# Performance work log

Hardware: AMD Instinct MI355X
Metric: run time of the kernel (lower is better)

Reference implementation:

```python
import jax, jax.numpy as jnp
import numpy as np

SHIFT = 1  # module's random shift_direction, fixed to +1 for determinism
B, C, H, W_SP = 1024, 512, 7, 7


def setup_inputs() -> dict:
    key = jax.random.key(0)
    k1, k2 = jax.random.split(key)
    x = jax.random.normal(k1, (B, C, H, W_SP), dtype=jnp.float32)
    W = jax.random.normal(k2, (256, 3, 3, 512), dtype=jnp.float32)
    return {"x": x, "W": W}


def _forward(x, W):
    # unfold along H with kernel (3,1), padding (1,0):
    # patches[b,c,kh,h,w] = x_padded[b,c,h+kh,w]
    xp = jnp.pad(x, ((0, 0), (0, 0), (1, 1), (0, 0)))
    t2 = jnp.stack([xp[:, :, k:k + H, :] for k in range(3)], axis=2)  # (B,512,3,7,7)
    # split channels 512 -> (2,256), move group dim next to H
    t2 = t2.reshape(B, 2, 256, 3, H, W_SP)
    t2 = t2.transpose(0, 2, 3, 4, 1, 5)          # (B,256,3,7,2,7)
    t2 = t2.reshape(B, 256, 3, 14, W_SP)         # interleave (h,group) -> 14
    t2 = jnp.roll(t2, SHIFT, axis=3)             # shift along interleaved dim
    t2 = t2.reshape(B, 256, 3, 7, 2, W_SP).sum(axis=4)  # (B,256,3,7,7)
    t2 = t2.transpose(0, 1, 3, 2, 4)             # (B,256,7,3,7) = (m,l,n,j,w)
    # second shift + unfold along w with kernel 3, padding 1
    t3 = jnp.roll(t2, SHIFT, axis=4)
    tp = jnp.pad(t3, ((0, 0), (0, 0), (0, 0), (0, 0), (1, 1)))
    t3u = jnp.stack([tp[..., k:k + W_SP] for k in range(3)], axis=4)  # (B,256,7,3,3,7) = (m,l,n,j,k,p)
    # torch einsum 'mlnjok, ljki -> mnoi' with o = output position, k = kernel tap
    out = jnp.einsum('mlnjkp,ljki->mpni', t3u, W)  # wait: check axis order below
    # Note: torch permutes (m,c,h,j,kernel,pos)->(m,c,h,j,pos,kernel) before einsum,
    # so contraction is over (l,j,kernel) and output is (m, n=h, o=pos, i).
    out = jnp.einsum('mlnjkp,ljki->mnpi', t3u, W)  # (B,7,7,512)
    return out.transpose(0, 3, 1, 2)              # (B,512,7,7)


def reference(x, W):
    return _forward(x, W)
```

## Files before the change

kernel.cpp:

```cpp
#include <hip/hip_runtime.h>
#include <hip/hip_bf16.h>


typedef __bf16 bf16x8 __attribute__((ext_vector_type(8)));
typedef float f32x4 __attribute__((ext_vector_type(4)));

#define VT_OFFSET (4u << 20)
#define VT_BYTES  (7168ull * 7 * 768 * 2)
#define WS_NEED   (VT_OFFSET + VT_BYTES)

__global__ __launch_bounds__(256) void prep_w(const float* __restrict__ Wg,
                                              __bf16* __restrict__ W2) {
    __shared__ float ws_[96][65];
    const int kt = blockIdx.x % 24;
    const int it_ = blockIdx.x / 24;
    const int K0 = kt * 96;
    const int I0 = it_ * 64;
    const int tid = threadIdx.x;

    #pragma unroll
    for (int t = 0; t < 6; ++t) {
        const int u = t * 256 + tid;
        const int row = u >> 4;
        const int f4 = u & 15;
        const float4 v = *(const float4*)(Wg + (size_t)(K0 + row) * 512 + I0 + f4 * 4);
        ws_[row][f4 * 4 + 0] = v.x;
        ws_[row][f4 * 4 + 1] = v.y;
        ws_[row][f4 * 4 + 2] = v.z;
        ws_[row][f4 * 4 + 3] = v.w;
    }
    __syncthreads();

    #pragma unroll
    for (int t = 0; t < 3; ++t) {
        const int u = t * 256 + tid;
        const int i = u / 12;
        const int rem = u - i * 12;
        const int tap = rem >> 2;
        const int q = rem & 3;
        bf16x8 o;
        #pragma unroll
        for (int e = 0; e < 8; ++e) {
            const int c_loc = q * 8 + e;
            o[e] = (__bf16)ws_[3 * c_loc + tap][i];
        }
        *(bf16x8*)(W2 + (size_t)(I0 + i) * 2304 + tap * 768 + 32 * kt + q * 8) = o;
    }
}

__global__ __launch_bounds__(256) void prep_v(const float* __restrict__ x,
                                              __bf16* __restrict__ Vt) {
    __shared__ float xs[256 * 49];
    const int b = blockIdx.x >> 1;
    const int g = blockIdx.x & 1;
    const int tid = threadIdx.x;

    {
        const float4* src0 = (const float4*)(x + ((size_t)b * 512 + g * 128) * 49);
        const float4* src1 = (const float4*)(x + ((size_t)b * 512 + 256 + g * 128) * 49);
        float4* dst0 = (float4*)xs;
        float4* dst1 = (float4*)(xs + 128 * 49);
        #pragma unroll
        for (int it = 0; it < 7; ++it) {
            const int q = it * 256 + tid;
            if (q < 1568) dst0[q] = src0[q];
        }
        #pragma unroll
        for (int it = 0; it < 7; ++it) {
            const int q = it * 256 + tid;
            if (q < 1568) dst1[q] = src1[q];
        }
    }
    __syncthreads();

    for (int h = 0; h < 7; ++h) {
        const int hm = (h + 6) % 7;
        for (int it = 0; it < 2; ++it) {
            const int u = it * 256 + tid;
            if (u < 336) {
                const int r = u / 48;
                const int k = u - r * 48;
                const int w = (r + 6) % 7;
                bf16x8 vv;
                #pragma unroll
                for (int e = 0; e < 8; ++e) {
                    const int c = k * 8 + e;
                    const int l = c / 3;
                    const int j = c - 3 * l;
                    const int r1 = h + j - 1;
                    const int r2 = hm + j - 1;
                    float v = 0.f;
                    if (r1 >= 0 && r1 < 7) v += xs[l * 49 + r1 * 7 + w];
                    if (r2 >= 0 && r2 < 7) v += xs[(128 + l) * 49 + r2 * 7 + w];
                    vv[e] = (__bf16)v;
                }
                *(bf16x8*)(Vt + (size_t)((b * 7 + h) * 7 + r) * 768 + g * 384 + k * 8) = vv;
            }
        }
    }
}

__global__ __launch_bounds__(256) void gemm_vt(const __bf16* __restrict__ Vt,
                                               const __bf16* __restrict__ W2,
                                               float* __restrict__ out) {
    __shared__ __bf16 T[16 * 400];
    __shared__ __bf16 Bt[128 * 104];

    const int tid = threadIdx.x;
    const int g0 = blockIdx.x;
    const int nb = (g0 >> 3) & 3;
    const int mb = ((g0 >> 5) << 3) | (g0 & 7);
    const int i0 = nb * 128;

    for (int q = tid; q < 3200; q += 256) ((int*)T)[q] = 0;

    const int lane = tid & 63;
    const int wave = tid >> 6;
    const int wm = wave >> 1;
    const int wn = wave & 1;
    const int ln15 = lane & 15;
    const int gq = lane >> 4;

    f32x4 acc[4][4];
    #pragma unroll
    for (int a = 0; a < 4; ++a)
        #pragma unroll
        for (int bq = 0; bq < 4; ++bq) acc[a][bq] = (f32x4){0.f, 0.f, 0.f, 0.f};

    __syncthreads();

    for (int chunk = 0; chunk < 24; ++chunk) {
        #pragma unroll
        for (int it = 0; it < 2; ++it) {
            const int u = it * 256 + tid;
            if (u < 448) {
                const int q = u & 3;
                const int tmp = u >> 2;
                const int t = tmp % 7;
                const int bh = tmp / 7;
                const float4 val = *(const float4*)(
                    Vt + (size_t)((mb * 16 + bh) * 7 + t) * 768 + chunk * 32 + q * 8);
                *(float4*)(&T[bh * 400 + (t + 1) * 40 + q * 8]) = val;
            }
        }
        #pragma unroll
        for (int it = 0; it < 6; ++it) {
            const int u = it * 256 + tid;
            const int tap = u >> 9;
            const int rem = u & 511;
            const int n = rem >> 2;
            const int q = rem & 3;
            const float4 val = *(const float4*)(W2 + (size_t)(i0 + n) * 2304 +
                                                tap * 768 + chunk * 32 + q * 8);
            *(float4*)(&Bt[n * 104 + tap * 32 + q * 8]) = val;
        }

        __syncthreads();

        #pragma unroll
        for (int tap = 0; tap < 3; ++tap) {
            bf16x8 af[4], bfr[4];
            #pragma unroll
            for (int mf = 0; mf < 4; ++mf) {
                const int bh_l = wm * 8 + mf * 2 + (ln15 >> 3);
                const int p = ln15 & 7;
                af[mf] = *(const bf16x8*)(&T[(bh_l * 10 + p + tap) * 40 + gq * 8]);
            }
            #pragma unroll
            for (int nf = 0; nf < 4; ++nf) {
                const int n_l = wn * 64 + nf * 16 + ln15;
                bfr[nf] = *(const bf16x8*)(&Bt[n_l * 104 + tap * 32 + gq * 8]);
            }
            #pragma unroll
            for (int mf = 0; mf < 4; ++mf)
                #pragma unroll
                for (int nf = 0; nf < 4; ++nf)
                    acc[mf][nf] = __builtin_amdgcn_mfma_f32_16x16x32_bf16(
                        af[mf], bfr[nf], acc[mf][nf], 0, 0, 0);
        }

        __syncthreads();
    }

    #pragma unroll
    for (int mf = 0; mf < 4; ++mf) {
        #pragma unroll
        for (int r = 0; r < 4; ++r) {
            const int mrow = gq * 4 + r;
            const int Mg_l = wm * 64 + mf * 16 + mrow;
            const int p = Mg_l & 7;
            if (p == 7) continue;
            const int bh_l = Mg_l >> 3;
            const int bhg = mb * 16 + bh_l;
            const int b = bhg / 7;
            const int h = bhg - 7 * b;
            #pragma unroll
            for (int nf = 0; nf < 4; ++nf) {
                const int i = i0 + wn * 64 + nf * 16 + ln15;
                out[(((size_t)b * 512 + i) * 7 + h) * 7 + p] = acc[mf][nf][r];
            }
        }
    }
}

__global__ __launch_bounds__(256) void gemm_shift(const float* __restrict__ x,
                                                  const __bf16* __restrict__ W2,
                                                  float* __restrict__ out) {
    __shared__ __bf16 T[16 * 10 * 40];
    __shared__ __bf16 Bt[128 * 104];

    const int tid = threadIdx.x;
    const int mb = blockIdx.x >> 2;
    const int nb = blockIdx.x & 3;
    const int i0 = nb * 128;

    const int cl  = tid & 31;
    const int bh0 = tid >> 5;
    const int bhg0 = mb * 16 + bh0;
    const int bhg1 = bhg0 + 8;
    const int b0 = bhg0 / 7, h0 = bhg0 - 7 * b0;
    const int b1 = bhg1 / 7, h1 = bhg1 - 7 * b1;
    const int hm0 = (h0 + 6) % 7, hm1 = (h1 + 6) % 7;

    for (int q = tid; q < 16 * 10 * 40 / 2; q += 256) ((int*)T)[q] = 0;

    const int lane = tid & 63;
    const int wave = tid >> 6;
    const int wm = wave >> 1;
    const int wn = wave & 1;
    const int ln15 = lane & 15;
    const int gq = lane >> 4;

    f32x4 acc[4][4];
    #pragma unroll
    for (int a = 0; a < 4; ++a)
        #pragma unroll
        for (int bq = 0; bq < 4; ++bq) acc[a][bq] = (f32x4){0.f, 0.f, 0.f, 0.f};

    __syncthreads();

    for (int chunk = 0; chunk < 24; ++chunk) {
        const int cg = chunk * 32 + cl;
        const int l = cg / 3;
        const int j = cg - 3 * l;
        {
            const int r1 = h0 + j - 1, r2 = hm0 + j - 1;
            float v[7] = {0.f, 0.f, 0.f, 0.f, 0.f, 0.f, 0.f};
            if (r1 >= 0 && r1 < 7) {
                const float* p1 = x + (((size_t)b0 * 512 + l) * 7 + r1) * 7;
                #pragma unroll
                for (int w = 0; w < 7; ++w) v[w] += p1[w];
            }
            if (r2 >= 0 && r2 < 7) {
                const float* p2 = x + (((size_t)b0 * 512 + 256 + l) * 7 + r2) * 7;
                #pragma unroll
                for (int w = 0; w < 7; ++w) v[w] += p2[w];
            }
            #pragma unroll
            for (int w = 0; w < 7; ++w)
                T[bh0 * 400 + ((w + 1) % 7 + 1) * 40 + cl] = (__bf16)v[w];
        }
        {
            const int r1 = h1 + j - 1, r2 = hm1 + j - 1;
            float v[7] = {0.f, 0.f, 0.f, 0.f, 0.f, 0.f, 0.f};
            if (r1 >= 0 && r1 < 7) {
                const float* p1 = x + (((size_t)b1 * 512 + l) * 7 + r1) * 7;
                #pragma unroll
                for (int w = 0; w < 7; ++w) v[w] += p1[w];
            }
            if (r2 >= 0 && r2 < 7) {
                const float* p2 = x + (((size_t)b1 * 512 + 256 + l) * 7 + r2) * 7;
                #pragma unroll
                for (int w = 0; w < 7; ++w) v[w] += p2[w];
            }
            #pragma unroll
            for (int w = 0; w < 7; ++w)
                T[(bh0 + 8) * 400 + ((w + 1) % 7 + 1) * 40 + cl] = (__bf16)v[w];
        }

        #pragma unroll
        for (int it = 0; it < 6; ++it) {
            const int u = it * 256 + tid;
            const int tap = u >> 9;
            const int rem = u & 511;
            const int n = rem >> 2;
            const int q = rem & 3;
            const float4 val = *(const float4*)(W2 + (size_t)(i0 + n) * 2304 +
                                                tap * 768 + chunk * 32 + q * 8);
            *(float4*)(&Bt[n * 104 + tap * 32 + q * 8]) = val;
        }

        __syncthreads();

        #pragma unroll
        for (int tap = 0; tap < 3; ++tap) {
            bf16x8 af[4], bfr[4];
            #pragma unroll
            for (int mf = 0; mf < 4; ++mf) {
                const int bh_l = wm * 8 + mf * 2 + (ln15 >> 3);
                const int p = ln15 & 7;
                af[mf] = *(const bf16x8*)(&T[(bh_l * 10 + p + tap) * 40 + gq * 8]);
            }
            #pragma unroll
            for (int nf = 0; nf < 4; ++nf) {
                const int n_l = wn * 64 + nf * 16 + ln15;
                bfr[nf] = *(const bf16x8*)(&Bt[n_l * 104 + tap * 32 + gq * 8]);
            }
            #pragma unroll
            for (int mf = 0; mf < 4; ++mf)
                #pragma unroll
                for (int nf = 0; nf < 4; ++nf)
                    acc[mf][nf] = __builtin_amdgcn_mfma_f32_16x16x32_bf16(
                        af[mf], bfr[nf], acc[mf][nf], 0, 0, 0);
        }

        __syncthreads();
    }

    #pragma unroll
    for (int mf = 0; mf < 4; ++mf) {
        #pragma unroll
        for (int r = 0; r < 4; ++r) {
            const int mrow = gq * 4 + r;
            const int Mg_l = wm * 64 + mf * 16 + mrow;
            const int p = Mg_l & 7;
            if (p == 7) continue;
            const int bh_l = Mg_l >> 3;
            const int bhg = mb * 16 + bh_l;
            const int b = bhg / 7;
            const int h = bhg - 7 * b;
            #pragma unroll
            for (int nf = 0; nf < 4; ++nf) {
                const int i = i0 + wn * 64 + nf * 16 + ln15;
                out[(((size_t)b * 512 + i) * 7 + h) * 7 + p] = acc[mf][nf][r];
            }
        }
    }
}

extern "C" void kernel_launch(void* const* d_in, const int* in_sizes, int n_in,
                              void* d_out, int out_size, void* d_ws, size_t ws_size,
                              hipStream_t stream) {
    const float* x  = (const float*)d_in[0];
    const float* Wg = (const float*)d_in[1];
    float* out = (float*)d_out;
    __bf16* W2 = (__bf16*)d_ws;

    prep_w<<<dim3(192), dim3(256), 0, stream>>>(Wg, W2);

    if (ws_size >= WS_NEED) {
        __bf16* Vt = (__bf16*)((char*)d_ws + VT_OFFSET);
        prep_v<<<dim3(2048), dim3(256), 0, stream>>>(x, Vt);
        gemm_vt<<<dim3(448 * 4), dim3(256), 0, stream>>>(Vt, W2, out);
    } else {
        gemm_shift<<<dim3(448 * 4), dim3(256), 0, stream>>>(x, W2, out);
    }
}
```

Baseline: 388.9 us.

## Double-buffer gemm_vt LDS tiles with direct global-to-LDS loads and XOR swizzle

Rewrites gemm_vt's main loop to stage the next K-chunk of activations and weights straight into LDS with global_load_lds while MFMAs run on the current buffer. One barrier per chunk now guards the double buffer instead of the load-then-compute sequence. Padding columns are replaced by an XOR swizzle to avoid bank conflicts, and out-of-range taps point to a shared zero region. LDS use rises to about 62 KB per block, which may lower occupancy, and the swizzle and offset math add correctness risk.

```diff
diff --git a/kernel.cpp b/kernel.cpp
--- a/kernel.cpp
+++ b/kernel.cpp
@@ -4,10 +4,17 @@
 
 typedef __bf16 bf16x8 __attribute__((ext_vector_type(8)));
 typedef float f32x4 __attribute__((ext_vector_type(4)));
+typedef unsigned int u32;
 
 #define VT_OFFSET (4u << 20)
 #define VT_BYTES  (7168ull * 7 * 768 * 2)
 #define WS_NEED   (VT_OFFSET + VT_BYTES)
+
+__device__ __forceinline__ void gload_lds16(const void* g, void* l) {
+    __builtin_amdgcn_global_load_lds(
+        (const __attribute__((address_space(1))) u32*)g,
+        (__attribute__((address_space(3))) u32*)l, 16, 0, 0);
+}
 
 __global__ __launch_bounds__(256) void prep_w(const float* __restrict__ Wg,
                                               __bf16* __restrict__ W2) {
@@ -103,8 +110,7 @@
 __global__ __launch_bounds__(256) void gemm_vt(const __bf16* __restrict__ Vt,
                                                const __bf16* __restrict__ W2,
                                                float* __restrict__ out) {
-    __shared__ __bf16 T[16 * 400];
-    __shared__ __bf16 Bt[128 * 104];
+    __shared__ __align__(1024) char L[63616];
 
     const int tid = threadIdx.x;
     const int g0 = blockIdx.x;
@@ -112,7 +118,34 @@
     const int mb = ((g0 >> 5) << 3) | (g0 & 7);
     const int i0 = nb * 128;
 
-    for (int q = tid; q < 3200; q += 256) ((int*)T)[q] = 0;
+    if (tid < 32) {
+        const int off = (tid < 16) ? 7168 + tid * 4 : 14400 + (tid - 16) * 4;
+        *(int*)(L + off) = 0;
+    }
+
+    int tsrc[2]; bool tok[2];
+    #pragma unroll
+    for (int it = 0; it < 2; ++it) {
+        const int u = it * 256 + tid;
+        tok[it] = (u < 448);
+        const int bh = u / 28;
+        const int rem = u - bh * 28;
+        const int ct = rem >> 2;
+        const int qs = rem & 3;
+        const int q = qs ^ (ct & 3);
+        tsrc[it] = ((mb * 16 + bh) * 7 + ct) * 1536 + q * 16;
+    }
+    int bsrc[6];
+    #pragma unroll
+    for (int it = 0; it < 6; ++it) {
+        const int s = it * 256 + tid;
+        const int tap = s >> 9;
+        const int rem = s & 511;
+        const int n = rem >> 2;
+        const int qs = rem & 3;
+        const int q = qs ^ ((n >> 1) & 3);
+        bsrc[it] = ((i0 + n) * 2304 + tap * 768 + q * 8) * 2;
+    }
 
     const int lane = tid & 63;
     const int wave = tid >> 6;
@@ -121,28 +154,172 @@
     const int ln15 = lane & 15;
     const int gq = lane >> 4;
 
+    int afoff[3][4], bfoff[3][4];
+    #pragma unroll
+    for (int tap = 0; tap < 3; ++tap) {
+        #pragma unroll
+        for (int mf = 0; mf < 4; ++mf) {
+            const int bh_l = wm * 8 + mf * 2 + (ln15 >> 3);
+            const int p = ln15 & 7;
+            const int ct = p + tap - 1;
+            afoff[tap][mf] = (ct >= 0 && ct <= 6)
+                ? bh_l * 448 + ct * 64 + ((gq ^ (ct & 3)) * 16)
+                : 7168;
+        }
+        #pragma unroll
+        for (int nf = 0; nf < 4; ++nf) {
+            const int n_l = wn * 64 + nf * 16 + ln15;
+            bfoff[tap][nf] = tap * 8192 + n_l * 64 + ((gq ^ ((n_l >> 1) & 3)) * 16);
+        }
+    }
+
     f32x4 acc[4][4];
     #pragma unroll
     for (int a = 0; a < 4; ++a)
         #pragma unroll
         for (int bq = 0; bq < 4; ++bq) acc[a][bq] = (f32x4){0.f, 0.f, 0.f, 0.f};
 
+    const char* VtB = (const char*)Vt;
+    const char* W2B = (const char*)W2;
+
+    auto stage = [&](int ck, int buf) {
+        const char* vb = VtB + ck * 64;
+        char* td = L + buf * 7232;
+        if (tok[0]) gload_lds16(vb + tsrc[0], td + tid * 16);
+        if (tok[1]) gload_lds16(vb + tsrc[1], td + 4096 + tid * 16);
+        const char* wb = W2B + ck * 64;
+        char* bd = L + 14464 + buf * 24576;
+        #pragma unroll
+        for (int it = 0; it < 6; ++it)
+            gload_lds16(wb + bsrc[it], bd + it * 4096 + tid * 16);
+    };
+
+    stage(0, 0);
     __syncthreads();
 
     for (int chunk = 0; chunk < 24; ++chunk) {
-        #pragma unroll
-        for (int it = 0; it < 2; ++it) {
-            const int u = it * 256 + tid;
-            if (u < 448) {
-                const int q = u & 3;
-                const int tmp = u >> 2;
-                const int t = tmp % 7;
-                const int bh = tmp / 7;
-                const float4 val = *(const float4*)(
-                    Vt + (size_t)((mb * 16 + bh) * 7 + t) * 768 + chunk * 32 + q * 8);
-                *(float4*)(&T[bh * 400 + (t + 1) * 40 + q * 8]) = val;
-            }
-        }
+        const int cur = chunk & 1;
+        if (chunk < 23) stage(chunk + 1, cur ^ 1);
+
+        const char* Tb = L + cur * 7232;
+        const char* Bb = L + 14464 + cur * 24576;
+
+        #pragma unroll
+        for (int tap = 0; tap < 3; ++tap) {
+            bf16x8 af[4], bfr[4];
+            #pragma unroll
+            for (int mf = 0; mf < 4; ++mf)
+                af[mf] = *(const bf16x8*)(Tb + afoff[tap][mf]);
+            #pragma unroll
+            for (int nf = 0; nf < 4; ++nf)
+                bfr[nf] = *(const bf16x8*)(Bb + bfoff[tap][nf]);
+            #pragma unroll
+            for (int mf = 0; mf < 4; ++mf)
+                #pragma unroll
+                for (int nf = 0; nf < 4; ++nf)
+                    acc[mf][nf] = __builtin_amdgcn_mfma_f32_16x16x32_bf16(
+                        af[mf], bfr[nf], acc[mf][nf], 0, 0, 0);
+        }
+
+        __syncthreads();
+    }
+
+    #pragma unroll
+    for (int mf = 0; mf < 4; ++mf) {
+        #pragma unroll
+        for (int r = 0; r < 4; ++r) {
+            const int mrow = gq * 4 + r;
+            const int Mg_l = wm * 64 + mf * 16 + mrow;
+            const int p = Mg_l & 7;
+            if (p == 7) continue;
+            const int bh_l = Mg_l >> 3;
+            const int bhg = mb * 16 + bh_l;
+            const int b = bhg / 7;
+            const int h = bhg - 7 * b;
+            #pragma unroll
+            for (int nf = 0; nf < 4; ++nf) {
+                const int i = i0 + wn * 64 + nf * 16 + ln15;
+                out[(((size_t)b * 512 + i) * 7 + h) * 7 + p] = acc[mf][nf][r];
+            }
+        }
+    }
+}
+
+__global__ __launch_bounds__(256) void gemm_shift(const float* __restrict__ x,
+                                                  const __bf16* __restrict__ W2,
+                                                  float* __restrict__ out) {
+    __shared__ __bf16 T[16 * 10 * 40];
+    __shared__ __bf16 Bt[128 * 104];
+
+    const int tid = threadIdx.x;
+    const int mb = blockIdx.x >> 2;
+    const int nb = blockIdx.x & 3;
+    const int i0 = nb * 128;
+
+    const int cl  = tid & 31;
+    const int bh0 = tid >> 5;
+    const int bhg0 = mb * 16 + bh0;
+    const int bhg1 = bhg0 + 8;
+    const int b0 = bhg0 / 7, h0 = bhg0 - 7 * b0;
+    const int b1 = bhg1 / 7, h1 = bhg1 - 7 * b1;
+    const int hm0 = (h0 + 6) % 7, hm1 = (h1 + 6) % 7;
+
+    for (int q = tid; q < 16 * 10 * 40 / 2; q += 256) ((int*)T)[q] = 0;
+
+    const int lane = tid & 63;
+    const int wave = tid >> 6;
+    const int wm = wave >> 1;
+    const int wn = wave & 1;
+    const int ln15 = lane & 15;
+    const int gq = lane >> 4;
+
+    f32x4 acc[4][4];
+    #pragma unroll
+    for (int a = 0; a < 4; ++a)
+        #pragma unroll
+        for (int bq = 0; bq < 4; ++bq) acc[a][bq] = (f32x4){0.f, 0.f, 0.f, 0.f};
+
+    __syncthreads();
+
+    for (int chunk = 0; chunk < 24; ++chunk) {
+        const int cg = chunk * 32 + cl;
+        const int l = cg / 3;
+        const int j = cg - 3 * l;
+        {
+            const int r1 = h0 + j - 1, r2 = hm0 + j - 1;
+            float v[7] = {0.f, 0.f, 0.f, 0.f, 0.f, 0.f, 0.f};
+            if (r1 >= 0 && r1 < 7) {
+                const float* p1 = x + (((size_t)b0 * 512 + l) * 7 + r1) * 7;
+                #pragma unroll
+                for (int w = 0; w < 7; ++w) v[w] += p1[w];
+            }
+            if (r2 >= 0 && r2 < 7) {
+                const float* p2 = x + (((size_t)b0 * 512 + 256 + l) * 7 + r2) * 7;
+                #pragma unroll
+                for (int w = 0; w < 7; ++w) v[w] += p2[w];
+            }
+            #pragma unroll
+            for (int w = 0; w < 7; ++w)
+                T[bh0 * 400 + ((w + 1) % 7 + 1) * 40 + cl] = (__bf16)v[w];
+        }
+        {
+            const int r1 = h1 + j - 1, r2 = hm1 + j - 1;
+            float v[7] = {0.f, 0.f, 0.f, 0.f, 0.f, 0.f, 0.f};
+            if (r1 >= 0 && r1 < 7) {
+                const float* p1 = x + (((size_t)b1 * 512 + l) * 7 + r1) * 7;
+                #pragma unroll
+                for (int w = 0; w < 7; ++w) v[w] += p1[w];
+            }
+            if (r2 >= 0 && r2 < 7) {
+                const float* p2 = x + (((size_t)b1 * 512 + 256 + l) * 7 + r2) * 7;
+                #pragma unroll
+                for (int w = 0; w < 7; ++w) v[w] += p2[w];
+            }
+            #pragma unroll
+            for (int w = 0; w < 7; ++w)
+                T[(bh0 + 8) * 400 + ((w + 1) % 7 + 1) * 40 + cl] = (__bf16)v[w];
+        }
+
         #pragma unroll
         for (int it = 0; it < 6; ++it) {
             const int u = it * 256 + tid;
@@ -203,141 +380,6 @@
     }
 }
 
-__global__ __launch_bounds__(256) void gemm_shift(const float* __restrict__ x,
-                                                  const __bf16* __restrict__ W2,
-                                                  float* __restrict__ out) {
-    __shared__ __bf16 T[16 * 10 * 40];
-    __shared__ __bf16 Bt[128 * 104];
-
-    const int tid = threadIdx.x;
-    const int mb = blockIdx.x >> 2;
-    const int nb = blockIdx.x & 3;
-    const int i0 = nb * 128;
-
-    const int cl  = tid & 31;
-    const int bh0 = tid >> 5;
-    const int bhg0 = mb * 16 + bh0;
-    const int bhg1 = bhg0 + 8;
-    const int b0 = bhg0 / 7, h0 = bhg0 - 7 * b0;
-    const int b1 = bhg1 / 7, h1 = bhg1 - 7 * b1;
-    const int hm0 = (h0 + 6) % 7, hm1 = (h1 + 6) % 7;
-
-    for (int q = tid; q < 16 * 10 * 40 / 2; q += 256) ((int*)T)[q] = 0;
-
-    const int lane = tid & 63;
-    const int wave = tid >> 6;
-    const int wm = wave >> 1;
-    const int wn = wave & 1;
-    const int ln15 = lane & 15;
-    const int gq = lane >> 4;
-
-    f32x4 acc[4][4];
-    #pragma unroll
-    for (int a = 0; a < 4; ++a)
-        #pragma unroll
-        for (int bq = 0; bq < 4; ++bq) acc[a][bq] = (f32x4){0.f, 0.f, 0.f, 0.f};
-
-    __syncthreads();
-
-    for (int chunk = 0; chunk < 24; ++chunk) {
-        const int cg = chunk * 32 + cl;
-        const int l = cg / 3;
-        const int j = cg - 3 * l;
-        {
-            const int r1 = h0 + j - 1, r2 = hm0 + j - 1;
-            float v[7] = {0.f, 0.f, 0.f, 0.f, 0.f, 0.f, 0.f};
-            if (r1 >= 0 && r1 < 7) {
-                const float* p1 = x + (((size_t)b0 * 512 + l) * 7 + r1) * 7;
-                #pragma unroll
-                for (int w = 0; w < 7; ++w) v[w] += p1[w];
-            }
-            if (r2 >= 0 && r2 < 7) {
-                const float* p2 = x + (((size_t)b0 * 512 + 256 + l) * 7 + r2) * 7;
-                #pragma unroll
-                for (int w = 0; w < 7; ++w) v[w] += p2[w];
-            }
-            #pragma unroll
-            for (int w = 0; w < 7; ++w)
-                T[bh0 * 400 + ((w + 1) % 7 + 1) * 40 + cl] = (__bf16)v[w];
-        }
-        {
-            const int r1 = h1 + j - 1, r2 = hm1 + j - 1;
-            float v[7] = {0.f, 0.f, 0.f, 0.f, 0.f, 0.f, 0.f};
-            if (r1 >= 0 && r1 < 7) {
-                const float* p1 = x + (((size_t)b1 * 512 + l) * 7 + r1) * 7;
-                #pragma unroll
-                for (int w = 0; w < 7; ++w) v[w] += p1[w];
-            }
-            if (r2 >= 0 && r2 < 7) {
-                const float* p2 = x + (((size_t)b1 * 512 + 256 + l) * 7 + r2) * 7;
-                #pragma unroll
-                for (int w = 0; w < 7; ++w) v[w] += p2[w];
-            }
-            #pragma unroll
-            for (int w = 0; w < 7; ++w)
-                T[(bh0 + 8) * 400 + ((w + 1) % 7 + 1) * 40 + cl] = (__bf16)v[w];
-        }
-
-        #pragma unroll
-        for (int it = 0; it < 6; ++it) {
-            const int u = it * 256 + tid;
-            const int tap = u >> 9;
-            const int rem = u & 511;
-            const int n = rem >> 2;
-            const int q = rem & 3;
-            const float4 val = *(const float4*)(W2 + (size_t)(i0 + n) * 2304 +
-                                                tap * 768 + chunk * 32 + q * 8);
-            *(float4*)(&Bt[n * 104 + tap * 32 + q * 8]) = val;
-        }
-
-        __syncthreads();
-
-        #pragma unroll
-        for (int tap = 0; tap < 3; ++tap) {
-            bf16x8 af[4], bfr[4];
-            #pragma unroll
-            for (int mf = 0; mf < 4; ++mf) {
-                const int bh_l = wm * 8 + mf * 2 + (ln15 >> 3);
-                const int p = ln15 & 7;
-                af[mf] = *(const bf16x8*)(&T[(bh_l * 10 + p + tap) * 40 + gq * 8]);
-            }
-            #pragma unroll
-            for (int nf = 0; nf < 4; ++nf) {
-                const int n_l = wn * 64 + nf * 16 + ln15;
-                bfr[nf] = *(const bf16x8*)(&Bt[n_l * 104 + tap * 32 + gq * 8]);
-            }
-            #pragma unroll
-            for (int mf = 0; mf < 4; ++mf)
-                #pragma unroll
-                for (int nf = 0; nf < 4; ++nf)
-                    acc[mf][nf] = __builtin_amdgcn_mfma_f32_16x16x32_bf16(
-                        af[mf], bfr[nf], acc[mf][nf], 0, 0, 0);
-        }
-
-        __syncthreads();
-    }
-
-    #pragma unroll
-    for (int mf = 0; mf < 4; ++mf) {
-        #pragma unroll
-        for (int r = 0; r < 4; ++r) {
-            const int mrow = gq * 4 + r;
-            const int Mg_l = wm * 64 + mf * 16 + mrow;
-            const int p = Mg_l & 7;
-            if (p == 7) continue;
-            const int bh_l = Mg_l >> 3;
-            const int bhg = mb * 16 + bh_l;
-            const int b = bhg / 7;
-            const int h = bhg - 7 * b;
-            #pragma unroll
-            for (int nf = 0; nf < 4; ++nf) {
-                const int i = i0 + wn * 64 + nf * 16 + ln15;
-                out[(((size_t)b * 512 + i) * 7 + h) * 7 + p] = acc[mf][nf][r];
-            }
-        }
-    }
-}
-
 extern "C" void kernel_launch(void* const* d_in, const int* in_sizes, int n_in,
                               void* d_out, int out_size, void* d_ws, size_t ws_size,
                               hipStream_t stream) {
```

New measurement: 358.4 us. 7.9% less time.
